# Kernel tuning notes

Hardware: AMD Instinct MI355X
Metric: run time of the kernel (lower is better)

The kernel has to match this reference:

```python
import jax, jax.numpy as jnp
import numpy as np

TEMPERATURE = 8.0  # sqrt(d_k=64)


def setup_inputs() -> dict:
    key = jax.random.key(0)
    ks = jax.random.split(key, 7)
    B, Lq, Lk, H, DK, DV, R, R2 = 4, 1024, 1024, 8, 64, 64, 32, 16
    return {
        "q":    jax.random.normal(ks[0], (B, Lq, H, DK), jnp.float32),
        "W_A":  jax.random.normal(ks[1], (H, DK, R),  jnp.float32) * 0.1,
        "W_B":  jax.random.normal(ks[2], (H, R, R2),  jnp.float32) * 0.1,
        "W_At": jax.random.normal(ks[3], (H, R, DK),  jnp.float32) * 0.1,
        "W_Bt": jax.random.normal(ks[4], (H, R2, R),  jnp.float32) * 0.1,
        "qt":   jax.random.normal(ks[5], (B, H, DK, Lk), jnp.float32),
        "v":    jax.random.normal(ks[6], (B, H, Lk, DV), jnp.float32),
        "d_k":  64,
        "mask": jnp.ones((B, 1, Lq, Lk), dtype=bool),
    }


def reference(q, W_A, W_B, W_At, W_Bt, qt, v, d_k, mask):
    # Low-rank projection chain: q -> A -> B -> Bt -> At  (per head b)
    IA      = jnp.einsum('kabc,bcd->kabd', q, W_A)        # [B,Lq,H,R]
    IAB     = jnp.einsum('kabj,bji->kabi', IA, W_B)       # [B,Lq,H,R2]
    IABBt   = jnp.einsum('kabi,bim->kabm', IAB, W_Bt)     # [B,Lq,H,R]
    IABBtAt = jnp.einsum('kabm,bmj->kabj', IABBt, W_At)   # [B,Lq,H,DK]
    # Bilinear score against transposed keys qt: [B,H,DK,Lk]
    attn = jnp.einsum('kabj,kbjm->kbam', IABBtAt, qt) / TEMPERATURE  # [B,H,Lq,Lk]
    attn = jnp.where(mask, attn, -1e9)
    attn = jax.nn.softmax(attn, axis=-1)
    # dropout p=0 (inference/reference) -> identity
    output = jnp.matmul(attn, v)  # [B,H,Lq,DV]
    return output, attn
```

## Files before the change

kernel.cpp:

```cpp
#include <hip/hip_runtime.h>

typedef short short8 __attribute__((ext_vector_type(8)));
typedef float f32x4 __attribute__((ext_vector_type(4)));

__device__ inline unsigned short f2bf(float f) {
    unsigned u = __builtin_bit_cast(unsigned, f);
    u += 0x7fff + ((u >> 16) & 1);
    return (unsigned short)(u >> 16);
}
__device__ inline short8 as_short8(uint4 v) { return __builtin_bit_cast(short8, v); }

__global__ void weff_kernel(const float* __restrict__ WA, const float* __restrict__ WB,
                            const float* __restrict__ WBt, const float* __restrict__ WAt,
                            float* __restrict__ Weff) {
    int h = blockIdx.x;
    int r = threadIdx.x;
    float wa[32];
#pragma unroll
    for (int c = 0; c < 32; ++c) wa[c] = WA[(h * 64 + r) * 32 + c];
    float t1[16];
#pragma unroll
    for (int i = 0; i < 16; ++i) {
        float s = 0.f;
#pragma unroll
        for (int c = 0; c < 32; ++c) s += wa[c] * WB[(h * 32 + c) * 16 + i];
        t1[i] = s;
    }
    float t2[32];
#pragma unroll
    for (int m = 0; m < 32; ++m) {
        float s = 0.f;
#pragma unroll
        for (int i = 0; i < 16; ++i) s += t1[i] * WBt[(h * 16 + i) * 32 + m];
        t2[m] = s;
    }
    for (int k = 0; k < 64; ++k) {
        float s = 0.f;
#pragma unroll
        for (int m = 0; m < 32; ++m) s += t2[m] * WAt[(h * 32 + m) * 64 + k];
        Weff[h * 4096 + r * 64 + k] = s;
    }
}

__global__ __launch_bounds__(256) void qp_kernel(const float* __restrict__ q,
                                                 const float* __restrict__ Weff,
                                                 unsigned short* __restrict__ Qp) {
    __shared__ float Wl[4096];
    __shared__ float qrow[4][64];
    int tid = threadIdx.x;
    int bh = blockIdx.x >> 8;
    int rb = (blockIdx.x & 255) * 4;
    int b = bh >> 3, h = bh & 7;
#pragma unroll
    for (int i = 0; i < 16; ++i) Wl[i * 256 + tid] = Weff[h * 4096 + i * 256 + tid];
    int rl = tid >> 6, k = tid & 63;
    qrow[rl][k] = q[((size_t)(b * 1024 + rb + rl) * 8 + h) * 64 + k];
    __syncthreads();
    float s = 0.f;
#pragma unroll
    for (int j = 0; j < 64; ++j) s += qrow[rl][j] * Wl[j * 64 + k];
    Qp[((size_t)bh * 1024 + rb + rl) * 64 + k] = f2bf(s * 0.125f);
}

__global__ __launch_bounds__(256) void qtp_kernel(const float* __restrict__ qt,
                                                  uint4* __restrict__ qtp) {
    int g = blockIdx.x * 256 + threadIdx.x;
    int lane = g & 63;
    int kc = (g >> 6) & 1;
    int nt = (g >> 7) & 63;
    int bh = g >> 13;
    int k = kc * 32 + (lane >> 4) * 8;
    int n = nt * 16 + (lane & 15);
    const float* src = qt + ((size_t)bh * 64 + k) * 1024 + n;
    unsigned short e[8];
#pragma unroll
    for (int j = 0; j < 8; ++j) e[j] = f2bf(src[(size_t)j * 1024]);
    uint4 o;
    o.x = e[0] | ((unsigned)e[1] << 16);
    o.y = e[2] | ((unsigned)e[3] << 16);
    o.z = e[4] | ((unsigned)e[5] << 16);
    o.w = e[6] | ((unsigned)e[7] << 16);
    qtp[g] = o;
}

__global__ __launch_bounds__(256) void vp_kernel(const float* __restrict__ v,
                                                 uint4* __restrict__ vp) {
    int g = blockIdx.x * 256 + threadIdx.x;
    int lane = g & 63;
    int kc = (g >> 6) & 31;
    int nt = (g >> 11) & 3;
    int bh = g >> 13;
    int k = kc * 32 + (lane >> 4) * 8;
    int n = nt * 16 + (lane & 15);
    const float* src = v + ((size_t)bh * 1024 + k) * 64 + n;
    unsigned short e[8];
#pragma unroll
    for (int j = 0; j < 8; ++j) e[j] = f2bf(src[(size_t)j * 64]);
    uint4 o;
    o.x = e[0] | ((unsigned)e[1] << 16);
    o.y = e[2] | ((unsigned)e[3] << 16);
    o.z = e[4] | ((unsigned)e[5] << 16);
    o.w = e[6] | ((unsigned)e[7] << 16);
    vp[g] = o;
}

__global__ __launch_bounds__(256, 2) void attn_kernel(
    const unsigned short* __restrict__ Qp,
    const uint4* __restrict__ qtp,
    const uint4* __restrict__ vp,
    float* __restrict__ outp,
    float* __restrict__ attnp) {
    constexpr int PST = 1032;
    __shared__ __align__(16) unsigned short Pbuf[32 * PST];
    __shared__ float redmax[2][2][16];
    __shared__ float redsum[2][2][16];
    __shared__ f32x4 outred[2][4][64];

    const int tid = threadIdx.x;
    const int wave = tid >> 6, lane = tid & 63;
    const int quad = lane >> 4, l16 = lane & 15;
    const int s = wave >> 1, c = wave & 1;
    const int bh = blockIdx.x >> 5;
    const int mblk = blockIdx.x & 31;

    const uint4* qpb = (const uint4*)(Qp + ((size_t)(bh * 1024 + mblk * 32 + s * 16 + l16)) * 64 + quad * 8);
    short8 a0 = as_short8(qpb[0]);
    short8 a1 = as_short8(qpb[4]);

    f32x4 acc[32];
    const uint4* qtb = qtp + (size_t)bh * 8192 + lane;
#pragma unroll
    for (int t = 0; t < 32; ++t) {
        int nt = c * 32 + t;
        uint4 b0 = qtb[(nt * 2 + 0) * 64];
        uint4 b1 = qtb[(nt * 2 + 1) * 64];
        f32x4 z = {0.f, 0.f, 0.f, 0.f};
        z = __builtin_amdgcn_mfma_f32_16x16x32_bf16(a0, as_short8(b0), z, 0, 0, 0);
        acc[t] = __builtin_amdgcn_mfma_f32_16x16x32_bf16(a1, as_short8(b1), z, 0, 0, 0);
    }

    float mx[4];
#pragma unroll
    for (int r = 0; r < 4; ++r) {
        float m = acc[0][r];
#pragma unroll
        for (int t = 1; t < 32; ++t) m = fmaxf(m, acc[t][r]);
#pragma unroll
        for (int off = 1; off < 16; off <<= 1) m = fmaxf(m, __shfl_xor(m, off, 64));
        mx[r] = m;
    }
    if (l16 == 0) {
        redmax[s][c][quad * 4 + 0] = mx[0];
        redmax[s][c][quad * 4 + 1] = mx[1];
        redmax[s][c][quad * 4 + 2] = mx[2];
        redmax[s][c][quad * 4 + 3] = mx[3];
    }
    __syncthreads();
    float rm[4];
#pragma unroll
    for (int r = 0; r < 4; ++r)
        rm[r] = fmaxf(redmax[s][0][quad * 4 + r], redmax[s][1][quad * 4 + r]);

    constexpr float LOG2E = 1.4426950408889634f;
    float sum[4] = {0.f, 0.f, 0.f, 0.f};
#pragma unroll
    for (int t = 0; t < 32; ++t) {
#pragma unroll
        for (int r = 0; r < 4; ++r) {
            float p = exp2f((acc[t][r] - rm[r]) * LOG2E);
            acc[t][r] = p;
            sum[r] += p;
        }
    }
#pragma unroll
    for (int r = 0; r < 4; ++r) {
#pragma unroll
        for (int off = 1; off < 16; off <<= 1) sum[r] += __shfl_xor(sum[r], off, 64);
    }
    if (l16 == 0) {
        redsum[s][c][quad * 4 + 0] = sum[0];
        redsum[s][c][quad * 4 + 1] = sum[1];
        redsum[s][c][quad * 4 + 2] = sum[2];
        redsum[s][c][quad * 4 + 3] = sum[3];
    }
    __syncthreads();
    float inv[4];
#pragma unroll
    for (int r = 0; r < 4; ++r)
        inv[r] = 1.0f / (redsum[s][0][quad * 4 + r] + redsum[s][1][quad * 4 + r]);

    size_t arowbase[4];
    int prowbase[4];
#pragma unroll
    for (int r = 0; r < 4; ++r) {
        int rowl = s * 16 + quad * 4 + r;
        arowbase[r] = ((size_t)bh * 1024 + mblk * 32 + rowl) * 1024 + c * 512 + l16;
        prowbase[r] = rowl * PST + c * 512 + l16;
    }
#pragma unroll
    for (int t = 0; t < 32; ++t) {
#pragma unroll
        for (int r = 0; r < 4; ++r) {
            float p = acc[t][r] * inv[r];
            attnp[arowbase[r] + t * 16] = p;
            Pbuf[prowbase[r] + t * 16] = f2bf(p);
        }
    }
    __syncthreads();

    f32x4 o[4];
#pragma unroll
    for (int nt = 0; nt < 4; ++nt) o[nt] = f32x4{0.f, 0.f, 0.f, 0.f};
    const uint4* vb = vp + (size_t)bh * 8192 + lane;
    const unsigned short* prow = &Pbuf[(s * 16 + l16) * PST + quad * 8];
#pragma unroll
    for (int kc = 0; kc < 16; ++kc) {
        int kg = c * 16 + kc;
        short8 a = as_short8(*(const uint4*)(prow + kg * 32));
#pragma unroll
        for (int nt = 0; nt < 4; ++nt) {
            uint4 b = vb[(nt * 32 + kg) * 64];
            o[nt] = __builtin_amdgcn_mfma_f32_16x16x32_bf16(a, as_short8(b), o[nt], 0, 0, 0);
        }
    }

    if (c == 1) {
#pragma unroll
        for (int nt = 0; nt < 4; ++nt) outred[s][nt][lane] = o[nt];
    }
    __syncthreads();
    if (c == 0) {
#pragma unroll
        for (int nt = 0; nt < 4; ++nt) {
            f32x4 o2 = outred[s][nt][lane];
#pragma unroll
            for (int r = 0; r < 4; ++r) {
                float val = o[nt][r] + o2[r];
                outp[((size_t)bh * 1024 + mblk * 32 + s * 16 + quad * 4 + r) * 64 + nt * 16 + l16] = val;
            }
        }
    }
}

extern "C" void kernel_launch(void* const* d_in, const int* in_sizes, int n_in,
                              void* d_out, int out_size, void* d_ws, size_t ws_size,
                              hipStream_t stream) {
    (void)in_sizes; (void)n_in; (void)out_size; (void)ws_size;
    const float* q   = (const float*)d_in[0];
    const float* WA  = (const float*)d_in[1];
    const float* WB  = (const float*)d_in[2];
    const float* WAt = (const float*)d_in[3];
    const float* WBt = (const float*)d_in[4];
    const float* qt  = (const float*)d_in[5];
    const float* v   = (const float*)d_in[6];

    float* outp  = (float*)d_out;
    float* attnp = outp + (size_t)4 * 8 * 1024 * 64;

    char* ws = (char*)d_ws;
    float* Weff          = (float*)ws;
    unsigned short* Qp   = (unsigned short*)(ws + 131072);
    uint4* qtp           = (uint4*)(ws + 131072 + 4194304);
    uint4* vp            = (uint4*)(ws + 131072 + 2 * 4194304);

    hipLaunchKernelGGL(qtp_kernel, dim3(1024), dim3(256), 0, stream, qt, qtp);
    hipLaunchKernelGGL(vp_kernel, dim3(1024), dim3(256), 0, stream, v, vp);
    hipLaunchKernelGGL(weff_kernel, dim3(8), dim3(64), 0, stream, WA, WB, WBt, WAt, Weff);
    hipLaunchKernelGGL(qp_kernel, dim3(8192), dim3(256), 0, stream, q, Weff, Qp);
    hipLaunchKernelGGL(attn_kernel, dim3(1024), dim3(256), 0, stream, Qp, qtp, vp, outp, attnp);
}
```

Measured before the change: 263.4 us.

## Shrink attention tile to 16 rows with four waves and merge repack kernels

The attention kernel now gives each block 16 query rows instead of 32. Its four waves each own a quarter of the key columns for the score and softmax step and a 16-wide slice of the value columns for P·V. This removes the cross-wave output reduction through shared memory, halves the P buffer, and raises the occupancy hint to 4 blocks per CU with twice as many blocks. The qt and v repack kernels are merged into one launch. In exchange, each block now re-reads all of V, and each wave's P·V loop is a serial chain of 32 MFMAs on a single accumulator.

```diff
diff --git a/kernel.cpp b/kernel.cpp
--- a/kernel.cpp
+++ b/kernel.cpp
@@ -62,76 +62,73 @@
     Qp[((size_t)bh * 1024 + rb + rl) * 64 + k] = f2bf(s * 0.125f);
 }
 
-__global__ __launch_bounds__(256) void qtp_kernel(const float* __restrict__ qt,
-                                                  uint4* __restrict__ qtp) {
+__global__ __launch_bounds__(256) void repack_kernel(const float* __restrict__ qt,
+                                                     const float* __restrict__ v,
+                                                     uint4* __restrict__ qtp,
+                                                     uint4* __restrict__ vp) {
     int g = blockIdx.x * 256 + threadIdx.x;
     int lane = g & 63;
-    int kc = (g >> 6) & 1;
-    int nt = (g >> 7) & 63;
-    int bh = g >> 13;
-    int k = kc * 32 + (lane >> 4) * 8;
-    int n = nt * 16 + (lane & 15);
-    const float* src = qt + ((size_t)bh * 64 + k) * 1024 + n;
+    const float* src;
+    uint4* dst;
+    size_t jstride;
+    if (g < 262144) {
+        int kc = (g >> 6) & 1;
+        int nt = (g >> 7) & 63;
+        int bh = g >> 13;
+        int k = kc * 32 + (lane >> 4) * 8;
+        int n = nt * 16 + (lane & 15);
+        src = qt + ((size_t)bh * 64 + k) * 1024 + n;
+        jstride = 1024;
+        dst = qtp + g;
+    } else {
+        int g2 = g - 262144;
+        int kc = (g2 >> 6) & 31;
+        int nt = (g2 >> 11) & 3;
+        int bh = g2 >> 13;
+        int k = kc * 32 + (lane >> 4) * 8;
+        int n = nt * 16 + (lane & 15);
+        src = v + ((size_t)bh * 1024 + k) * 64 + n;
+        jstride = 64;
+        dst = vp + g2;
+    }
     unsigned short e[8];
 #pragma unroll
-    for (int j = 0; j < 8; ++j) e[j] = f2bf(src[(size_t)j * 1024]);
+    for (int j = 0; j < 8; ++j) e[j] = f2bf(src[jstride * j]);
     uint4 o;
     o.x = e[0] | ((unsigned)e[1] << 16);
     o.y = e[2] | ((unsigned)e[3] << 16);
     o.z = e[4] | ((unsigned)e[5] << 16);
     o.w = e[6] | ((unsigned)e[7] << 16);
-    qtp[g] = o;
-}
-
-__global__ __launch_bounds__(256) void vp_kernel(const float* __restrict__ v,
-                                                 uint4* __restrict__ vp) {
-    int g = blockIdx.x * 256 + threadIdx.x;
-    int lane = g & 63;
-    int kc = (g >> 6) & 31;
-    int nt = (g >> 11) & 3;
-    int bh = g >> 13;
-    int k = kc * 32 + (lane >> 4) * 8;
-    int n = nt * 16 + (lane & 15);
-    const float* src = v + ((size_t)bh * 1024 + k) * 64 + n;
-    unsigned short e[8];
-#pragma unroll
-    for (int j = 0; j < 8; ++j) e[j] = f2bf(src[(size_t)j * 64]);
-    uint4 o;
-    o.x = e[0] | ((unsigned)e[1] << 16);
-    o.y = e[2] | ((unsigned)e[3] << 16);
-    o.z = e[4] | ((unsigned)e[5] << 16);
-    o.w = e[6] | ((unsigned)e[7] << 16);
-    vp[g] = o;
-}
-
-__global__ __launch_bounds__(256, 2) void attn_kernel(
+    *dst = o;
+}
+
+__global__ __launch_bounds__(256, 4) void attn_kernel(
     const unsigned short* __restrict__ Qp,
     const uint4* __restrict__ qtp,
     const uint4* __restrict__ vp,
     float* __restrict__ outp,
     float* __restrict__ attnp) {
     constexpr int PST = 1032;
-    __shared__ __align__(16) unsigned short Pbuf[32 * PST];
-    __shared__ float redmax[2][2][16];
-    __shared__ float redsum[2][2][16];
-    __shared__ f32x4 outred[2][4][64];
+    __shared__ __align__(16) unsigned short Pbuf[16 * PST];
+    __shared__ float redmax[4][16];
+    __shared__ float redsum[4][16];
 
     const int tid = threadIdx.x;
-    const int wave = tid >> 6, lane = tid & 63;
+    const int w = tid >> 6, lane = tid & 63;
     const int quad = lane >> 4, l16 = lane & 15;
-    const int s = wave >> 1, c = wave & 1;
-    const int bh = blockIdx.x >> 5;
-    const int mblk = blockIdx.x & 31;
-
-    const uint4* qpb = (const uint4*)(Qp + ((size_t)(bh * 1024 + mblk * 32 + s * 16 + l16)) * 64 + quad * 8);
+    const int bh = blockIdx.x >> 6;
+    const int mblk = blockIdx.x & 63;
+    const int rowbase = bh * 1024 + mblk * 16;
+
+    const uint4* qpb = (const uint4*)(Qp + ((size_t)(rowbase + l16)) * 64 + quad * 8);
     short8 a0 = as_short8(qpb[0]);
     short8 a1 = as_short8(qpb[4]);
 
-    f32x4 acc[32];
+    f32x4 acc[16];
     const uint4* qtb = qtp + (size_t)bh * 8192 + lane;
 #pragma unroll
-    for (int t = 0; t < 32; ++t) {
-        int nt = c * 32 + t;
+    for (int t = 0; t < 16; ++t) {
+        int nt = w * 16 + t;
         uint4 b0 = qtb[(nt * 2 + 0) * 64];
         uint4 b1 = qtb[(nt * 2 + 1) * 64];
         f32x4 z = {0.f, 0.f, 0.f, 0.f};
@@ -139,32 +136,26 @@
         acc[t] = __builtin_amdgcn_mfma_f32_16x16x32_bf16(a1, as_short8(b1), z, 0, 0, 0);
     }
 
-    float mx[4];
 #pragma unroll
     for (int r = 0; r < 4; ++r) {
         float m = acc[0][r];
 #pragma unroll
-        for (int t = 1; t < 32; ++t) m = fmaxf(m, acc[t][r]);
+        for (int t = 1; t < 16; ++t) m = fmaxf(m, acc[t][r]);
 #pragma unroll
         for (int off = 1; off < 16; off <<= 1) m = fmaxf(m, __shfl_xor(m, off, 64));
-        mx[r] = m;
-    }
-    if (l16 == 0) {
-        redmax[s][c][quad * 4 + 0] = mx[0];
-        redmax[s][c][quad * 4 + 1] = mx[1];
-        redmax[s][c][quad * 4 + 2] = mx[2];
-        redmax[s][c][quad * 4 + 3] = mx[3];
+        if (l16 == 0) redmax[w][quad * 4 + r] = m;
     }
     __syncthreads();
     float rm[4];
 #pragma unroll
     for (int r = 0; r < 4; ++r)
-        rm[r] = fmaxf(redmax[s][0][quad * 4 + r], redmax[s][1][quad * 4 + r]);
+        rm[r] = fmaxf(fmaxf(redmax[0][quad * 4 + r], redmax[1][quad * 4 + r]),
+                      fmaxf(redmax[2][quad * 4 + r], redmax[3][quad * 4 + r]));
 
     constexpr float LOG2E = 1.4426950408889634f;
     float sum[4] = {0.f, 0.f, 0.f, 0.f};
 #pragma unroll
-    for (int t = 0; t < 32; ++t) {
+    for (int t = 0; t < 16; ++t) {
 #pragma unroll
         for (int r = 0; r < 4; ++r) {
             float p = exp2f((acc[t][r] - rm[r]) * LOG2E);
@@ -176,70 +167,40 @@
     for (int r = 0; r < 4; ++r) {
 #pragma unroll
         for (int off = 1; off < 16; off <<= 1) sum[r] += __shfl_xor(sum[r], off, 64);
-    }
-    if (l16 == 0) {
-        redsum[s][c][quad * 4 + 0] = sum[0];
-        redsum[s][c][quad * 4 + 1] = sum[1];
-        redsum[s][c][quad * 4 + 2] = sum[2];
-        redsum[s][c][quad * 4 + 3] = sum[3];
+        if (l16 == 0) redsum[w][quad * 4 + r] = sum[r];
     }
     __syncthreads();
     float inv[4];
 #pragma unroll
     for (int r = 0; r < 4; ++r)
-        inv[r] = 1.0f / (redsum[s][0][quad * 4 + r] + redsum[s][1][quad * 4 + r]);
-
-    size_t arowbase[4];
-    int prowbase[4];
-#pragma unroll
-    for (int r = 0; r < 4; ++r) {
-        int rowl = s * 16 + quad * 4 + r;
-        arowbase[r] = ((size_t)bh * 1024 + mblk * 32 + rowl) * 1024 + c * 512 + l16;
-        prowbase[r] = rowl * PST + c * 512 + l16;
-    }
-#pragma unroll
-    for (int t = 0; t < 32; ++t) {
+        inv[r] = 1.0f / (redsum[0][quad * 4 + r] + redsum[1][quad * 4 + r] +
+                         redsum[2][quad * 4 + r] + redsum[3][quad * 4 + r]);
+
+    float* abase = attnp + (size_t)rowbase * 1024 + w * 256 + l16;
+#pragma unroll
+    for (int t = 0; t < 16; ++t) {
 #pragma unroll
         for (int r = 0; r < 4; ++r) {
+            int rowl = quad * 4 + r;
             float p = acc[t][r] * inv[r];
-            attnp[arowbase[r] + t * 16] = p;
-            Pbuf[prowbase[r] + t * 16] = f2bf(p);
+            abase[rowl * 1024 + t * 16] = p;
+            Pbuf[rowl * PST + w * 256 + t * 16 + l16] = f2bf(p);
         }
     }
     __syncthreads();
 
-    f32x4 o[4];
-#pragma unroll
-    for (int nt = 0; nt < 4; ++nt) o[nt] = f32x4{0.f, 0.f, 0.f, 0.f};
-    const uint4* vb = vp + (size_t)bh * 8192 + lane;
-    const unsigned short* prow = &Pbuf[(s * 16 + l16) * PST + quad * 8];
-#pragma unroll
-    for (int kc = 0; kc < 16; ++kc) {
-        int kg = c * 16 + kc;
-        short8 a = as_short8(*(const uint4*)(prow + kg * 32));
-#pragma unroll
-        for (int nt = 0; nt < 4; ++nt) {
-            uint4 b = vb[(nt * 32 + kg) * 64];
-            o[nt] = __builtin_amdgcn_mfma_f32_16x16x32_bf16(a, as_short8(b), o[nt], 0, 0, 0);
-        }
-    }
-
-    if (c == 1) {
-#pragma unroll
-        for (int nt = 0; nt < 4; ++nt) outred[s][nt][lane] = o[nt];
-    }
-    __syncthreads();
-    if (c == 0) {
-#pragma unroll
-        for (int nt = 0; nt < 4; ++nt) {
-            f32x4 o2 = outred[s][nt][lane];
-#pragma unroll
-            for (int r = 0; r < 4; ++r) {
-                float val = o[nt][r] + o2[r];
-                outp[((size_t)bh * 1024 + mblk * 32 + s * 16 + quad * 4 + r) * 64 + nt * 16 + l16] = val;
-            }
-        }
-    }
+    f32x4 o = {0.f, 0.f, 0.f, 0.f};
+    const uint4* vb = vp + (size_t)bh * 8192 + (size_t)w * 32 * 64 + lane;
+    const unsigned short* prow = &Pbuf[l16 * PST + quad * 8];
+#pragma unroll
+    for (int kc = 0; kc < 32; ++kc) {
+        short8 a = as_short8(*(const uint4*)(prow + kc * 32));
+        uint4 b = vb[kc * 64];
+        o = __builtin_amdgcn_mfma_f32_16x16x32_bf16(a, as_short8(b), o, 0, 0, 0);
+    }
+#pragma unroll
+    for (int r = 0; r < 4; ++r)
+        outp[((size_t)(rowbase + quad * 4 + r)) * 64 + w * 16 + l16] = o[r];
 }
 
 extern "C" void kernel_launch(void* const* d_in, const int* in_sizes, int n_in,
@@ -263,9 +224,8 @@
     uint4* qtp           = (uint4*)(ws + 131072 + 4194304);
     uint4* vp            = (uint4*)(ws + 131072 + 2 * 4194304);
 
-    hipLaunchKernelGGL(qtp_kernel, dim3(1024), dim3(256), 0, stream, qt, qtp);
-    hipLaunchKernelGGL(vp_kernel, dim3(1024), dim3(256), 0, stream, v, vp);
+    hipLaunchKernelGGL(repack_kernel, dim3(2048), dim3(256), 0, stream, qt, v, qtp, vp);
     hipLaunchKernelGGL(weff_kernel, dim3(8), dim3(64), 0, stream, WA, WB, WBt, WAt, Weff);
     hipLaunchKernelGGL(qp_kernel, dim3(8192), dim3(256), 0, stream, q, Weff, Qp);
-    hipLaunchKernelGGL(attn_kernel, dim3(1024), dim3(256), 0, stream, Qp, qtp, vp, outp, attnp);
-}
+    hipLaunchKernelGGL(attn_kernel, dim3(2048), dim3(256), 0, stream, Qp, qtp, vp, outp, attnp);
+}
```

Result: faster. 251.0 us (-4.7%).
